# Optimization experiments

Hardware: AMD Instinct MI355X
Metric: run time of the kernel (lower is better)

## Reference

```python
import jax, jax.numpy as jnp
import numpy as np

BS, HIST, H, W, NOBJ = 512, 3, 10, 10, 4
NSENT, TOK, DM = 3, 36, 768
EMB, FM, K, NL, ADIM = 256, 64, 2, 128, 5
LIN = FM * (H - (K - 1)) * (W - (K - 1))  # 64*9*9 = 5184
ATTN_SCALE = float(np.sqrt(EMB))  # 16.0


def setup_inputs() -> dict:
    key = jax.random.key(0)
    ks = jax.random.split(key, 24)
    g = lambda i, shape, s=0.02: jax.random.normal(ks[i], shape, dtype=jnp.float32) * s
    sprite_emb = g(0, (25, EMB), 1.0).at[0].set(0.0)  # padding_idx=0 -> zero row
    inp = {
        'state': jax.random.randint(ks[1], (BS, HIST, H, W, NOBJ), 0, 25, dtype=jnp.int32),
        'action': jax.random.randint(ks[2], (BS,), 0, ADIM, dtype=jnp.int32),
        'temb': jax.random.normal(ks[3], (BS, NSENT, TOK, DM), dtype=jnp.float32),
        'sprite_emb': sprite_emb,
        'conv_w': g(4, (K, K, HIST * EMB, FM)),  # HWIO
        'conv_b': g(5, (FM,)),
        'Wk': g(6, (DM, EMB)), 'bk': g(7, (EMB,)),
        'Wks': g(8, (DM, 1)), 'bks': g(9, (1,)),
        'Wv': g(10, (DM, EMB)), 'bv': g(11, (EMB,)),
        'Wvs': g(12, (DM, 1)), 'bvs': g(13, (1,)),
        'a1': g(14, (LIN, NL)), 'a1b': g(15, (NL,)),
        'a2': g(16, (NL, NL)), 'a2b': g(17, (NL,)),
        'a3': g(18, (NL, ADIM)), 'a3b': g(19, (ADIM,)),
        'v1': g(20, (LIN, NL)), 'v1b': g(21, (NL,)),
        'v2': g(22, (NL, NL)), 'v2b': g(23, (NL,)),
        'v3': jax.random.normal(jax.random.fold_in(key, 99), (NL, 1)) * 0.02,
        'v3b': jnp.zeros((1,), jnp.float32),
    }
    return inp


def _nonzero_mean(e):
    # e: [..., n, emb]; mean over rows that are nonzero (padding rows are all-zero)
    cnt = jnp.sum(jnp.sum(e, axis=-1) != 0, axis=-1, keepdims=True)
    return jnp.sum(e, axis=-2) / jnp.maximum(cnt, 1).astype(e.dtype)


def reference(state, action, temb, sprite_emb, conv_w, conv_b, Wk, bk, Wks, bks,
              Wv, bv, Wvs, bvs, a1, a1b, a2, a2b, a3, a3b, v1, v1b, v2, v2b, v3, v3b):
    lrelu = jax.nn.leaky_relu  # slope 0.01 matches torch default
    bs = state.shape[0]
    obj_state, avt_state = state[..., :-1], state[..., -1:]
    query = _nonzero_mean(sprite_emb[obj_state])   # [bs,hist,H,W,emb]
    avatar = _nonzero_mean(sprite_emb[avt_state])  # [bs,hist,H,W,emb]
    # text key/value: scaled token-softmax pooling over tokens (dim=2)
    k = (temb @ Wk + bk) * jax.nn.softmax(temb @ Wks + bks, axis=-2)
    k = jnp.sum(k, axis=2)                          # [bs,nsent,emb]
    v = (temb @ Wv + bv) * jax.nn.softmax(temb @ Wvs + bvs, axis=-2)
    v = jnp.sum(v, axis=2)                          # [bs,nsent,emb]
    # batch_attention
    q2 = query.reshape(bs, -1, EMB)                 # [bs, hist*H*W, emb]
    kq = jnp.einsum('bxe,bse->bxs', q2, k) / ATTN_SCALE
    wts = jax.nn.softmax(kq, axis=-1) * (kq != 0)
    wts = wts.reshape(bs, HIST, H, W, NSENT)
    # mean(weights[...,None]*value, dim=-2) == (w @ v) / nsent
    att = jnp.einsum('bthws,bse->bthwe', wts, v) / NSENT  # [bs,hist,H,W,emb]
    st = att.reshape(bs, H, W, -1)                  # fold hist into channels (768)
    av = avatar.reshape(bs, H, W, -1)
    st = (st + av) / 2.0                            # NHWC, C=768
    y = jax.lax.conv_general_dilated(st, conv_w, (1, 1), 'VALID',
                                     dimension_numbers=('NHWC', 'HWIO', 'NHWC')) + conv_b
    y = lrelu(y)                                    # [bs,9,9,64]
    y = jnp.transpose(y, (0, 3, 1, 2)).reshape(bs, -1)  # torch NCHW flatten order
    ha = lrelu(lrelu(y @ a1 + a1b) @ a2 + a2b)
    logits = ha @ a3 + a3b
    logp = jax.nn.log_softmax(logits, axis=-1)
    action_logprobs = jnp.take_along_axis(logp, action[:, None].astype(jnp.int32), axis=-1)[:, 0]
    entropy = -jnp.sum(jnp.exp(logp) * logp, axis=-1)
    hv = lrelu(lrelu(y @ v1 + v1b) @ v2 + v2b)
    state_value = (hv @ v3 + v3b)[:, 0]
    return action_logprobs, state_value, entropy
```

## Files before the change

kernel.cpp:

```cpp
#include <hip/hip_runtime.h>
#include <hip/hip_bf16.h>
#include <math.h>

constexpr int BS   = 512;
constexpr int DM   = 768;
constexpr int NBS  = 1536;
constexpr int NPOS = 300;
constexpr int LIN  = 5184;
constexpr int KSPLIT = 9, KCH = 576;
constexpr int NROW = 55296;

typedef __attribute__((ext_vector_type(8))) short bf16x8;
typedef __attribute__((ext_vector_type(4))) short s16x4;
typedef __attribute__((ext_vector_type(4))) float f32x4;

static __device__ __forceinline__ short f2bf(float f) {
    unsigned u = __float_as_uint(f);
    unsigned r = (u + 0x7FFFu + ((u >> 16) & 1u)) >> 16;
    return (short)r;
}
static __device__ __forceinline__ float bf2f_lo(unsigned u) { return __uint_as_float(u << 16); }
static __device__ __forceinline__ float bf2f_hi(unsigned u) { return __uint_as_float(u & 0xFFFF0000u); }

constexpr size_t OFF_RD   = 0;
constexpr size_t OFF_FL   = 19968;
constexpr size_t OFF_DT   = 20032;
constexpr size_t OFF_W2T  = 118336;
constexpr size_t OFF_WVH  = 167488;
constexpr size_t OFF_WCT  = 216640;
constexpr size_t OFF_PH   = 511552;
constexpr size_t OFF_AB   = 536128;
constexpr size_t OFF_SK   = 1199680;
constexpr size_t OFF_SV   = 1254976;
constexpr size_t OFF_XKH  = 1310272;
constexpr size_t OFF_XVH  = 1900096;
constexpr size_t OFF_VWH  = 2489920;
constexpr size_t OFF_YH   = 3079744;
constexpr size_t OFF_PART = 4406848;

__global__ __launch_bounds__(256) void k1_scores_prep(
    const float* __restrict__ temb, const float* __restrict__ Wks,
    const float* __restrict__ Wvs, const float* __restrict__ conv_w,
    const float* __restrict__ sprite, const float* __restrict__ Wk,
    const float* __restrict__ Wv, const float* __restrict__ bv,
    const float* __restrict__ a1, const float* __restrict__ v1,
    float* __restrict__ SK, float* __restrict__ SV,
    short* __restrict__ W2T, short* __restrict__ WVH, short* __restrict__ AB,
    short* __restrict__ PH, float* __restrict__ RD, int* __restrict__ FL)
{
    __shared__ float tile[64][65];
    int tid = threadIdx.x, bx = blockIdx.x;

    if (bx < 13824) {
        int wid = tid >> 6, lane = tid & 63;
        size_t r = (size_t)bx * 4 + wid;
        const float4* row = (const float4*)temb + r * 192;
        const float4* k4 = (const float4*)Wks;
        const float4* v4 = (const float4*)Wvs;
        float pk = 0.f, pv = 0.f;
        #pragma unroll
        for (int i = 0; i < 3; ++i) {
            int d4 = lane + 64 * i;
            float4 x = row[d4];
            float4 wk = k4[d4], wv = v4[d4];
            pk += x.x * wk.x + x.y * wk.y + x.z * wk.z + x.w * wk.w;
            pv += x.x * wv.x + x.y * wv.y + x.z * wv.z + x.w * wv.w;
        }
        #pragma unroll
        for (int off = 32; off; off >>= 1) {
            pk += __shfl_down(pk, off);
            pv += __shfl_down(pv, off);
        }
        if (lane == 0) { SK[r] = pk; SV[r] = pv; }
        return;
    }

    int id = bx - 13824;
    if (id < 48) {
        int p = id >> 2, cq = id & 3;
        int t4 = p / 3, j = p - t4 * 3;
        int c0 = cq * 64;
        #pragma unroll
        for (int it = 0; it < 16; ++it) {
            int idx = it * 256 + tid; int ci = idx >> 6, f = idx & 63;
            tile[ci][f] = conv_w[(size_t)(t4 * 768 + j * 256 + c0 + ci) * 64 + f];
        }
        __syncthreads();
        #pragma unroll
        for (int it = 0; it < 16; ++it) {
            int idx = it * 256 + tid; int f = idx >> 6, ci = idx & 63;
            W2T[(size_t)((t4 * 3 + j) * 64 + f) * 256 + c0 + ci] = f2bf(tile[ci][f]);
        }
    } else if (id < 96) {
        int b2 = id - 48;
        int base = b2 * 4096 + tid * 16;
        #pragma unroll
        for (int q = 0; q < 4; ++q) {
            float4 v = *(const float4*)(Wv + base + q * 4);
            s16x4 h = { f2bf(v.x), f2bf(v.y), f2bf(v.z), f2bf(v.w) };
            *(s16x4*)(WVH + base + q * 4) = h;
        }
    } else if (id < 420) {
        int q = id - 96; int kt = q % 81, nt = q / 81;
        const float* src = (nt < 2) ? a1 : v1;
        int col0 = (nt & 1) * 64;
        #pragma unroll
        for (int it = 0; it < 16; ++it) {
            int idx = it * 256 + tid; int ki = idx >> 6, ni = idx & 63;
            tile[ki][ni] = src[(size_t)(kt * 64 + ki) * 128 + col0 + ni];
        }
        __syncthreads();
        #pragma unroll
        for (int it = 0; it < 16; ++it) {
            int idx = it * 256 + tid; int ni = idx >> 6, ki = idx & 63;
            AB[(size_t)(nt * 64 + ni) * 5184 + kt * 64 + ki] = f2bf(tile[ki][ni]);
        }
    } else if (id < 495) {
        int g = (id - 420) * 256 + tid;
        int o = g / 768, d = g - o * 768;
        const float* sp = sprite + o * 256;
        const float* wr = Wk + (size_t)d * 256;
        float s = 0.f;
        for (int c = 0; c < 256; ++c) s += sp[c] * wr[c];
        PH[(size_t)o * 768 + d] = f2bf(s);
    } else if (id < 573) {
        int g = (id - 495) * 256 + tid;
        int o = g / 768, n = g - o * 768;
        int tap = n >> 6, f = n & 63; int t4 = tap / 3, j = tap - t4 * 3;
        const float* sp = (o < 25) ? (sprite + o * 256) : bv;
        float s = 0.f;
        for (int e = 0; e < 256; ++e)
            s += sp[e] * conv_w[(size_t)(t4 * 768 + j * 256 + e) * 64 + f];
        RD[g] = s;
    } else {
        if (tid < 25) {
            float s = 0.f;
            for (int c = 0; c < 256; ++c) s += sprite[tid * 256 + c];
            FL[tid] = (s != 0.0f) ? 1 : 0;
        }
    }
}

__global__ __launch_bounds__(384) void kB2_sum(
    const float* __restrict__ temb, const float* __restrict__ SK,
    const float* __restrict__ SV, short* __restrict__ XKH, short* __restrict__ XVH)
{
    __shared__ float swk[40], swv[40];
    int tid = threadIdx.x, bs = blockIdx.x;
    int wid = tid >> 6, lane = tid & 63;

    if (wid < 2) {
        const float* S = wid ? SV : SK;
        float s = (lane < 36) ? S[(size_t)bs * 36 + lane] : -INFINITY;
        float m = s;
        #pragma unroll
        for (int off = 32; off; off >>= 1) m = fmaxf(m, __shfl_xor(m, off));
        float e = (lane < 36) ? expf(s - m) : 0.f;
        float z = e;
        #pragma unroll
        for (int off = 32; off; off >>= 1) z += __shfl_xor(z, off);
        float* dst = wid ? swv : swk;
        if (lane < 36) dst[lane] = e / z;
    }
    __syncthreads();

    const float2* row = (const float2*)(temb + (size_t)bs * 27648);
    float k0 = 0.f, k1 = 0.f, v0 = 0.f, v1 = 0.f;
    #pragma unroll
    for (int t = 0; t < 36; ++t) {
        float2 x = row[(size_t)t * 384 + tid];
        float wk = swk[t], wv = swv[t];
        k0 += wk * x.x; k1 += wk * x.y;
        v0 += wv * x.x; v1 += wv * x.y;
    }
    ushort2 hk = { (unsigned short)f2bf(k0), (unsigned short)f2bf(k1) };
    ushort2 hv = { (unsigned short)f2bf(v0), (unsigned short)f2bf(v1) };
    *(ushort2*)&XKH[(size_t)bs * 768 + 2 * tid] = hk;
    *(ushort2*)&XVH[(size_t)bs * 768 + 2 * tid] = hv;
}

template<int BIAS, int OUTBF>
__global__ __launch_bounds__(256) void gemm_mfma(
    const short* __restrict__ A, const short* __restrict__ B,
    const float* __restrict__ bias, void* __restrict__ Cout,
    int K, int ldc, int klen, size_t czstride)
{
    __shared__ short As[64][40];
    __shared__ short Bs[64][40];
    int tid = threadIdx.x;
    int bm = blockIdx.x * 64, bn = blockIdx.y * 64;
    int wid = tid >> 6, lane = tid & 63;
    int wm = (wid >> 1) * 32, wn = (wid & 1) * 32;
    int l15 = lane & 15, lg = lane >> 4;

    f32x4 zero = {0.f, 0.f, 0.f, 0.f};
    f32x4 acc00 = zero, acc01 = zero, acc10 = zero, acc11 = zero;

    int srow = tid >> 2, kch = (tid & 3) * 8;
    const short* Ap = A + (size_t)(bm + srow) * K + kch + (size_t)blockIdx.z * klen;
    const short* Bp = B + (size_t)(bn + srow) * K + kch + (size_t)blockIdx.z * klen;

    for (int kt = 0; kt < klen; kt += 32) {
        bf16x8 aval = *(const bf16x8*)(Ap + kt);
        bf16x8 bval = *(const bf16x8*)(Bp + kt);
        *(bf16x8*)&As[srow][kch] = aval;
        *(bf16x8*)&Bs[srow][kch] = bval;
        __syncthreads();
        bf16x8 af0 = *(const bf16x8*)&As[wm + l15][lg * 8];
        bf16x8 af1 = *(const bf16x8*)&As[wm + 16 + l15][lg * 8];
        bf16x8 bg0 = *(const bf16x8*)&Bs[wn + l15][lg * 8];
        bf16x8 bg1 = *(const bf16x8*)&Bs[wn + 16 + l15][lg * 8];
        acc00 = __builtin_amdgcn_mfma_f32_16x16x32_bf16(af0, bg0, acc00, 0, 0, 0);
        acc01 = __builtin_amdgcn_mfma_f32_16x16x32_bf16(af0, bg1, acc01, 0, 0, 0);
        acc10 = __builtin_amdgcn_mfma_f32_16x16x32_bf16(af1, bg0, acc10, 0, 0, 0);
        acc11 = __builtin_amdgcn_mfma_f32_16x16x32_bf16(af1, bg1, acc11, 0, 0, 0);
        __syncthreads();
    }

    float* Cf = (float*)Cout + (size_t)blockIdx.z * czstride;
    short* Ch = (short*)Cout;
    #pragma unroll
    for (int i = 0; i < 2; ++i) {
        f32x4 arow0 = (i == 0) ? acc00 : acc10;
        f32x4 arow1 = (i == 0) ? acc01 : acc11;
        #pragma unroll
        for (int j = 0; j < 2; ++j) {
            f32x4 a = (j == 0) ? arow0 : arow1;
            int col = bn + wn + j * 16 + l15;
            float bb = BIAS ? bias[col] : 0.f;
            #pragma unroll
            for (int r = 0; r < 4; ++r) {
                int row = bm + wm + i * 16 + lg * 4 + r;
                float v = a[r] + bb;
                if (OUTBF) Ch[(size_t)row * ldc + col] = f2bf(v);
                else       Cf[(size_t)row * ldc + col] = v;
            }
        }
    }
}

__global__ __launch_bounds__(256) void k3_vwdt(
    const short* __restrict__ XVH, const short* __restrict__ WCT,
    const float* __restrict__ bvW2, short* __restrict__ VWH,
    const short* __restrict__ XKH, const short* __restrict__ PH,
    float* __restrict__ DT)
{
    __shared__ short As[64][40];
    __shared__ short Bs[64][40];
    int tid = threadIdx.x;
    bool isdt = (blockIdx.y == 12);
    const short* A = isdt ? XKH : XVH;
    const short* B = isdt ? PH  : WCT;
    int bm = blockIdx.x * 64, bn = isdt ? 0 : blockIdx.y * 64;
    int wid = tid >> 6, lane = tid & 63;
    int wm = (wid >> 1) * 32, wn = (wid & 1) * 32;
    int l15 = lane & 15, lg = lane >> 4;

    f32x4 zero = {0.f, 0.f, 0.f, 0.f};
    f32x4 acc00 = zero, acc01 = zero, acc10 = zero, acc11 = zero;

    int srow = tid >> 2, kch = (tid & 3) * 8;
    const short* Ap = A + (size_t)(bm + srow) * 768 + kch;
    const short* Bp = B + (size_t)(bn + srow) * 768 + kch;

    for (int kt = 0; kt < 768; kt += 32) {
        bf16x8 aval = *(const bf16x8*)(Ap + kt);
        bf16x8 bval = *(const bf16x8*)(Bp + kt);
        *(bf16x8*)&As[srow][kch] = aval;
        *(bf16x8*)&Bs[srow][kch] = bval;
        __syncthreads();
        bf16x8 af0 = *(const bf16x8*)&As[wm + l15][lg * 8];
        bf16x8 af1 = *(const bf16x8*)&As[wm + 16 + l15][lg * 8];
        bf16x8 bg0 = *(const bf16x8*)&Bs[wn + l15][lg * 8];
        bf16x8 bg1 = *(const bf16x8*)&Bs[wn + 16 + l15][lg * 8];
        acc00 = __builtin_amdgcn_mfma_f32_16x16x32_bf16(af0, bg0, acc00, 0, 0, 0);
        acc01 = __builtin_amdgcn_mfma_f32_16x16x32_bf16(af0, bg1, acc01, 0, 0, 0);
        acc10 = __builtin_amdgcn_mfma_f32_16x16x32_bf16(af1, bg0, acc10, 0, 0, 0);
        acc11 = __builtin_amdgcn_mfma_f32_16x16x32_bf16(af1, bg1, acc11, 0, 0, 0);
        __syncthreads();
    }

    #pragma unroll
    for (int i = 0; i < 2; ++i) {
        f32x4 arow0 = (i == 0) ? acc00 : acc10;
        f32x4 arow1 = (i == 0) ? acc01 : acc11;
        #pragma unroll
        for (int j = 0; j < 2; ++j) {
            f32x4 a = (j == 0) ? arow0 : arow1;
            int col = bn + wn + j * 16 + l15;
            #pragma unroll
            for (int r = 0; r < 4; ++r) {
                int row = bm + wm + i * 16 + lg * 4 + r;
                if (isdt) DT[(size_t)row * 64 + col] = a[r];
                else      VWH[(size_t)row * 768 + col] = f2bf(a[r] + bvW2[col]);
            }
        }
    }
}

__global__ __launch_bounds__(512) void k4_y(
    const int* __restrict__ state, const float* __restrict__ dt,
    const int* __restrict__ flags, const short* __restrict__ VWH,
    const float* __restrict__ rowdot, const float* __restrict__ conv_b,
    short* __restrict__ y)
{
    int b = blockIdx.x, tid = threadIdx.x;
    __shared__ float s_vW[3 * 768];
    __shared__ float s_w[3][NPOS + 4];
    __shared__ int   s_avt[NPOS + 4];
    __shared__ float s_y[81 * 65];

    const unsigned* vr = (const unsigned*)(VWH + (size_t)b * 3 * 768);
    for (int i = tid; i < 1152; i += 512) {
        unsigned u = vr[i];
        s_vW[2 * i]     = bf2f_lo(u);
        s_vW[2 * i + 1] = bf2f_hi(u);
    }

    for (int code = tid; code < NPOS; code += 512) {
        const int* st = state + ((size_t)b * NPOS + code) * 4;
        int o0 = st[0], o1 = st[1], o2 = st[2], avi = st[3];
        int cnt = flags[o0] + flags[o1] + flags[o2];
        s_avt[code] = avi;
        float w0 = 0.f, w1 = 0.f, w2 = 0.f;
        if (cnt > 0) {
            const float* d0 = dt + (size_t)b * 192;
            float inv = 1.0f / (16.0f * (float)cnt);
            float q0 = (d0[o0]       + d0[o1]       + d0[o2])       * inv;
            float q1 = (d0[64 + o0]  + d0[64 + o1]  + d0[64 + o2])  * inv;
            float q2 = (d0[128 + o0] + d0[128 + o1] + d0[128 + o2]) * inv;
            float m = fmaxf(q0, fmaxf(q1, q2));
            float e0 = expf(q0 - m), e1 = expf(q1 - m), e2 = expf(q2 - m);
            float is = 1.0f / (6.0f * (e0 + e1 + e2));
            w0 = e0 * is; w1 = e1 * is; w2 = e2 * is;
        }
        s_w[0][code] = w0; s_w[1][code] = w1; s_w[2][code] = w2;
    }
    __syncthreads();

    int f = tid & 63;
    float cb = conv_b[f];
    for (int p = tid >> 6; p < 81; p += 8) {
        int oh = p / 9, ow = p - oh * 9;
        float acc = cb;
        #pragma unroll
        for (int kh = 0; kh < 2; ++kh)
        #pragma unroll
        for (int kw = 0; kw < 2; ++kw) {
            int bc = 3 * ((oh + kh) * 10 + (ow + kw));
            int tbase = ((kh * 2 + kw) * 3) * 64 + f;
            #pragma unroll
            for (int j = 0; j < 3; ++j) {
                int code = bc + j;
                int tf = tbase + j * 64;
                acc += s_w[0][code] * s_vW[tf]
                     + s_w[1][code] * s_vW[768 + tf]
                     + s_w[2][code] * s_vW[2 * 768 + tf];
                acc += 0.5f * rowdot[(size_t)s_avt[code] * 768 + tf];
            }
        }
        acc = acc > 0.f ? acc : 0.01f * acc;
        s_y[p * 65 + f] = acc;
    }
    __syncthreads();
    for (int i = tid; i < LIN; i += 512) {
        int ff = i / 81, pp = i - ff * 81;
        y[(size_t)b * LIN + i] = f2bf(s_y[pp * 65 + ff]);
    }
}

__global__ __launch_bounds__(128) void k6_heads(
    const float* __restrict__ PART, const float* __restrict__ a1b,
    const float* __restrict__ v1b, const int* __restrict__ action,
    const float* __restrict__ a2, const float* __restrict__ a2b,
    const float* __restrict__ a3, const float* __restrict__ a3b,
    const float* __restrict__ v2, const float* __restrict__ v2b,
    const float* __restrict__ v3, const float* __restrict__ v3b,
    float* __restrict__ out)
{
    int b = blockIdx.x, tid = threadIdx.x;
    __shared__ float h1a[128], h1v[128], h2a[128], red[128];
    __shared__ float lg[5];
    float sa0 = a1b[tid], sv0 = v1b[tid];
    const float* pb = PART + (size_t)b * 256;
    for (int z = 0; z < KSPLIT; ++z) {
        sa0 += pb[(size_t)z * (BS * 256) + tid];
        sv0 += pb[(size_t)z * (BS * 256) + 128 + tid];
    }
    h1a[tid] = sa0 > 0.f ? sa0 : 0.01f * sa0;
    h1v[tid] = sv0 > 0.f ? sv0 : 0.01f * sv0;
    __syncthreads();
    float sa = a2b[tid], sv = v2b[tid];
    for (int k = 0; k < 128; ++k) {
        sa += h1a[k] * a2[k * 128 + tid];
        sv += h1v[k] * v2[k * 128 + tid];
    }
    sa = sa > 0.f ? sa : 0.01f * sa;
    sv = sv > 0.f ? sv : 0.01f * sv;
    h2a[tid] = sa;
    red[tid] = sv * v3[tid];
    __syncthreads();
    for (int s = 64; s > 0; s >>= 1) {
        if (tid < s) red[tid] += red[tid + s];
        __syncthreads();
    }
    if (tid < 5) {
        float l = a3b[tid];
        for (int k = 0; k < 128; ++k) l += h2a[k] * a3[k * 5 + tid];
        lg[tid] = l;
    }
    __syncthreads();
    if (tid == 0) {
        float m = lg[0];
        for (int j2 = 1; j2 < 5; ++j2) m = fmaxf(m, lg[j2]);
        float se = 0.f;
        for (int j2 = 0; j2 < 5; ++j2) se += expf(lg[j2] - m);
        float lse = m + logf(se);
        int act = action[b];
        float ent = 0.f;
        for (int j2 = 0; j2 < 5; ++j2) {
            float lp = lg[j2] - lse;
            ent -= expf(lp) * lp;
        }
        out[b]        = lg[act] - lse;
        out[512 + b]  = red[0] + v3b[0];
        out[1024 + b] = ent;
    }
}

extern "C" void kernel_launch(void* const* d_in, const int* in_sizes, int n_in,
                              void* d_out, int out_size, void* d_ws, size_t ws_size,
                              hipStream_t stream)
{
    const int*   state  = (const int*)d_in[0];
    const int*   action = (const int*)d_in[1];
    const float* temb   = (const float*)d_in[2];
    const float* sprite = (const float*)d_in[3];
    const float* conv_w = (const float*)d_in[4];
    const float* conv_b = (const float*)d_in[5];
    const float* Wk     = (const float*)d_in[6];
    const float* Wks    = (const float*)d_in[8];
    const float* Wv     = (const float*)d_in[10];
    const float* bv     = (const float*)d_in[11];
    const float* Wvs    = (const float*)d_in[12];
    const float* a1     = (const float*)d_in[14];
    const float* a1b    = (const float*)d_in[15];
    const float* a2     = (const float*)d_in[16];
    const float* a2b    = (const float*)d_in[17];
    const float* a3     = (const float*)d_in[18];
    const float* a3b    = (const float*)d_in[19];
    const float* v1     = (const float*)d_in[20];
    const float* v1b    = (const float*)d_in[21];
    const float* v2     = (const float*)d_in[22];
    const float* v2b    = (const float*)d_in[23];
    const float* v3     = (const float*)d_in[24];
    const float* v3b    = (const float*)d_in[25];
    (void)in_sizes; (void)n_in; (void)out_size; (void)ws_size;

    float* ws  = (float*)d_ws;
    float* RD  = ws + OFF_RD;
    float* bvW2= RD + 25 * 768;
    int*   FL  = (int*)(ws + OFF_FL);
    float* DT  = ws + OFF_DT;
    short* W2T = (short*)(ws + OFF_W2T);
    short* WVH = (short*)(ws + OFF_WVH);
    short* WCT = (short*)(ws + OFF_WCT);
    short* PH  = (short*)(ws + OFF_PH);
    short* AB  = (short*)(ws + OFF_AB);
    float* SK  = ws + OFF_SK;
    float* SV  = ws + OFF_SV;
    short* XKH = (short*)(ws + OFF_XKH);
    short* XVH = (short*)(ws + OFF_XVH);
    short* VWH = (short*)(ws + OFF_VWH);
    short* YH  = (short*)(ws + OFF_YH);
    float* PART= ws + OFF_PART;
    float* out = (float*)d_out;

    k1_scores_prep<<<13824 + 574, 256, 0, stream>>>(
        temb, Wks, Wvs, conv_w, sprite, Wk, Wv, bv, a1, v1,
        SK, SV, W2T, WVH, AB, PH, RD, FL);
    kB2_sum<<<NBS, 384, 0, stream>>>(temb, SK, SV, XKH, XVH);
    gemm_mfma<0,1><<<dim3(12,12,1),256,0,stream>>>(W2T, WVH, nullptr, WCT, 256, 768, 256, 0);
    k3_vwdt<<<dim3(24,13,1),256,0,stream>>>(XVH, WCT, bvW2, VWH, XKH, PH, DT);
    k4_y<<<BS, 512, 0, stream>>>(state, DT, FL, VWH, RD, conv_b, YH);
    gemm_mfma<0,0><<<dim3(8,4,KSPLIT),256,0,stream>>>(YH, AB, nullptr, PART, 5184, 256, KCH, (size_t)BS*256);
    k6_heads<<<BS, 128, 0, stream>>>(PART, a1b, v1b, action, a2, a2b, a3, a3b,
                                     v2, v2b, v3, v3b, out);
}
```

Baseline: 131.0 us.

## Fold conv-weight x Wv product into prep kernel and split softmax from token sum

Drops the separate bf16 transpose and cast of conv_w and Wv and the small MFMA GEMM that formed WCT. WCT is now computed directly in fp32 by extra blocks of the prep kernel using an LDS-tiled scalar GEMM, which removes one launch and two staging buffers. The token softmax moves into its own small kernel that writes the weights to global memory. The token-weighted sum then uses float4 loads over 192 threads with batched loads. This trades one launch for another and replaces MFMA with scalar FMA for WCT, which could lengthen the tail of the prep kernel.

```diff
diff --git a/kernel.cpp b/kernel.cpp
--- a/kernel.cpp
+++ b/kernel.cpp
@@ -3,15 +3,12 @@
 #include <math.h>
 
 constexpr int BS   = 512;
-constexpr int DM   = 768;
 constexpr int NBS  = 1536;
 constexpr int NPOS = 300;
 constexpr int LIN  = 5184;
 constexpr int KSPLIT = 9, KCH = 576;
-constexpr int NROW = 55296;
 
 typedef __attribute__((ext_vector_type(8))) short bf16x8;
-typedef __attribute__((ext_vector_type(4))) short s16x4;
 typedef __attribute__((ext_vector_type(4))) float f32x4;
 
 static __device__ __forceinline__ short f2bf(float f) {
@@ -19,34 +16,37 @@
     unsigned r = (u + 0x7FFFu + ((u >> 16) & 1u)) >> 16;
     return (short)r;
 }
+static __device__ __forceinline__ unsigned pk2(float a, float b) {
+    return ((unsigned)(unsigned short)f2bf(a)) | (((unsigned)(unsigned short)f2bf(b)) << 16);
+}
 static __device__ __forceinline__ float bf2f_lo(unsigned u) { return __uint_as_float(u << 16); }
 static __device__ __forceinline__ float bf2f_hi(unsigned u) { return __uint_as_float(u & 0xFFFF0000u); }
 
 constexpr size_t OFF_RD   = 0;
 constexpr size_t OFF_FL   = 19968;
 constexpr size_t OFF_DT   = 20032;
-constexpr size_t OFF_W2T  = 118336;
-constexpr size_t OFF_WVH  = 167488;
-constexpr size_t OFF_WCT  = 216640;
-constexpr size_t OFF_PH   = 511552;
-constexpr size_t OFF_AB   = 536128;
-constexpr size_t OFF_SK   = 1199680;
-constexpr size_t OFF_SV   = 1254976;
-constexpr size_t OFF_XKH  = 1310272;
-constexpr size_t OFF_XVH  = 1900096;
-constexpr size_t OFF_VWH  = 2489920;
-constexpr size_t OFF_YH   = 3079744;
-constexpr size_t OFF_PART = 4406848;
-
-__global__ __launch_bounds__(256) void k1_scores_prep(
+constexpr size_t OFF_WCT  = 118336;
+constexpr size_t OFF_PH   = 413248;
+constexpr size_t OFF_AB   = 437824;
+constexpr size_t OFF_SK   = 1101376;
+constexpr size_t OFF_SV   = 1156672;
+constexpr size_t OFF_SWK  = 1211968;
+constexpr size_t OFF_SWV  = 1267264;
+constexpr size_t OFF_XKH  = 1322560;
+constexpr size_t OFF_XVH  = 1912384;
+constexpr size_t OFF_VWH  = 2502208;
+constexpr size_t OFF_YH   = 3092032;
+constexpr size_t OFF_PART = 4419136;
+
+__global__ __launch_bounds__(256) void kS_scores_prep(
     const float* __restrict__ temb, const float* __restrict__ Wks,
     const float* __restrict__ Wvs, const float* __restrict__ conv_w,
     const float* __restrict__ sprite, const float* __restrict__ Wk,
     const float* __restrict__ Wv, const float* __restrict__ bv,
     const float* __restrict__ a1, const float* __restrict__ v1,
     float* __restrict__ SK, float* __restrict__ SV,
-    short* __restrict__ W2T, short* __restrict__ WVH, short* __restrict__ AB,
-    short* __restrict__ PH, float* __restrict__ RD, int* __restrict__ FL)
+    short* __restrict__ AB, short* __restrict__ PH, short* __restrict__ WCT,
+    float* __restrict__ RD, int* __restrict__ FL)
 {
     __shared__ float tile[64][65];
     int tid = threadIdx.x, bx = blockIdx.x;
@@ -76,32 +76,8 @@
     }
 
     int id = bx - 13824;
-    if (id < 48) {
-        int p = id >> 2, cq = id & 3;
-        int t4 = p / 3, j = p - t4 * 3;
-        int c0 = cq * 64;
-        #pragma unroll
-        for (int it = 0; it < 16; ++it) {
-            int idx = it * 256 + tid; int ci = idx >> 6, f = idx & 63;
-            tile[ci][f] = conv_w[(size_t)(t4 * 768 + j * 256 + c0 + ci) * 64 + f];
-        }
-        __syncthreads();
-        #pragma unroll
-        for (int it = 0; it < 16; ++it) {
-            int idx = it * 256 + tid; int f = idx >> 6, ci = idx & 63;
-            W2T[(size_t)((t4 * 3 + j) * 64 + f) * 256 + c0 + ci] = f2bf(tile[ci][f]);
-        }
-    } else if (id < 96) {
-        int b2 = id - 48;
-        int base = b2 * 4096 + tid * 16;
-        #pragma unroll
-        for (int q = 0; q < 4; ++q) {
-            float4 v = *(const float4*)(Wv + base + q * 4);
-            s16x4 h = { f2bf(v.x), f2bf(v.y), f2bf(v.z), f2bf(v.w) };
-            *(s16x4*)(WVH + base + q * 4) = h;
-        }
-    } else if (id < 420) {
-        int q = id - 96; int kt = q % 81, nt = q / 81;
+    if (id < 324) {
+        int kt = id % 81, nt = id / 81;
         const float* src = (nt < 2) ? a1 : v1;
         int col0 = (nt & 1) * 64;
         #pragma unroll
@@ -115,23 +91,70 @@
             int idx = it * 256 + tid; int ni = idx >> 6, ki = idx & 63;
             AB[(size_t)(nt * 64 + ni) * 5184 + kt * 64 + ki] = f2bf(tile[ki][ni]);
         }
-    } else if (id < 495) {
-        int g = (id - 420) * 256 + tid;
-        int o = g / 768, d = g - o * 768;
-        const float* sp = sprite + o * 256;
-        const float* wr = Wk + (size_t)d * 256;
-        float s = 0.f;
-        for (int c = 0; c < 256; ++c) s += sp[c] * wr[c];
-        PH[(size_t)o * 768 + d] = f2bf(s);
-    } else if (id < 573) {
-        int g = (id - 495) * 256 + tid;
-        int o = g / 768, n = g - o * 768;
-        int tap = n >> 6, f = n & 63; int t4 = tap / 3, j = tap - t4 * 3;
-        const float* sp = (o < 25) ? (sprite + o * 256) : bv;
-        float s = 0.f;
-        for (int e = 0; e < 256; ++e)
-            s += sp[e] * conv_w[(size_t)(t4 * 768 + j * 256 + e) * 64 + f];
-        RD[g] = s;
+    } else if (id < 399) {
+        int g = (id - 324) * 256 + tid;
+        if (g < 19200) {
+            int o = g / 768, d = g - o * 768;
+            const float* sp = sprite + o * 256;
+            const float* wr = Wk + (size_t)d * 256;
+            float s = 0.f;
+            for (int c = 0; c < 256; ++c) s += sp[c] * wr[c];
+            PH[(size_t)o * 768 + d] = f2bf(s);
+        }
+    } else if (id < 477) {
+        int g = (id - 399) * 256 + tid;
+        if (g < 19968) {
+            int o = g / 768, n = g - o * 768;
+            int tap = n >> 6, f = n & 63; int t4 = tap / 3, j = tap - t4 * 3;
+            const float* sp = (o < 25) ? (sprite + o * 256) : bv;
+            float s = 0.f;
+            for (int e = 0; e < 256; ++e)
+                s += sp[e] * conv_w[(size_t)(t4 * 768 + j * 256 + e) * 64 + f];
+            RD[g] = s;
+        }
+    } else if (id < 621) {
+        int wid2 = id - 477;
+        int bm = (wid2 / 12) * 64, bn = (wid2 % 12) * 64;
+        int p = bm >> 6; int t4 = p / 3, jj = p - t4 * 3;
+        const float* cwb = conv_w + (size_t)(t4 * 768 + jj * 256) * 64;
+        float* As = (float*)tile;
+        float* Bs = (float*)tile + 2080;
+        float acc[4][4];
+        #pragma unroll
+        for (int i = 0; i < 4; ++i)
+            #pragma unroll
+            for (int j = 0; j < 4; ++j) acc[i][j] = 0.f;
+        int tm = tid >> 4, tn = tid & 15;
+        for (int kc = 0; kc < 256; kc += 32) {
+            #pragma unroll
+            for (int it = 0; it < 8; ++it) {
+                int idx = it * 256 + tid; int c = idx >> 6, f = idx & 63;
+                As[c * 65 + f] = cwb[(size_t)(kc + c) * 64 + f];
+            }
+            #pragma unroll
+            for (int it = 0; it < 8; ++it) {
+                int idx = it * 256 + tid; int d = idx >> 5, c = idx & 31;
+                Bs[c * 65 + d] = Wv[(size_t)(bn + d) * 256 + kc + c];
+            }
+            __syncthreads();
+            for (int kk = 0; kk < 32; ++kk) {
+                float a[4], b[4];
+                #pragma unroll
+                for (int i = 0; i < 4; ++i) a[i] = As[kk * 65 + tm * 4 + i];
+                #pragma unroll
+                for (int j = 0; j < 4; ++j) b[j] = Bs[kk * 65 + tn * 4 + j];
+                #pragma unroll
+                for (int i = 0; i < 4; ++i)
+                    #pragma unroll
+                    for (int j = 0; j < 4; ++j) acc[i][j] += a[i] * b[j];
+            }
+            __syncthreads();
+        }
+        #pragma unroll
+        for (int i = 0; i < 4; ++i)
+            #pragma unroll
+            for (int j = 0; j < 4; ++j)
+                WCT[(size_t)(bm + tm * 4 + i) * 768 + bn + tn * 4 + j] = f2bf(acc[i][j]);
     } else {
         if (tid < 25) {
             float s = 0.f;
@@ -141,17 +164,14 @@
     }
 }
 
-__global__ __launch_bounds__(384) void kB2_sum(
-    const float* __restrict__ temb, const float* __restrict__ SK,
-    const float* __restrict__ SV, short* __restrict__ XKH, short* __restrict__ XVH)
-{
-    __shared__ float swk[40], swv[40];
-    int tid = threadIdx.x, bs = blockIdx.x;
-    int wid = tid >> 6, lane = tid & 63;
-
-    if (wid < 2) {
-        const float* S = wid ? SV : SK;
-        float s = (lane < 36) ? S[(size_t)bs * 36 + lane] : -INFINITY;
+__global__ __launch_bounds__(512) void kW_weights(
+    const float* __restrict__ SK, const float* __restrict__ SV,
+    float* __restrict__ SWK, float* __restrict__ SWV)
+{
+    int w = threadIdx.x >> 6, lane = threadIdx.x & 63;
+    int bs = blockIdx.x * 8 + w;
+    {
+        float s = (lane < 36) ? SK[(size_t)bs * 36 + lane] : -1e30f;
         float m = s;
         #pragma unroll
         for (int off = 32; off; off >>= 1) m = fmaxf(m, __shfl_xor(m, off));
@@ -159,24 +179,53 @@
         float z = e;
         #pragma unroll
         for (int off = 32; off; off >>= 1) z += __shfl_xor(z, off);
-        float* dst = wid ? swv : swk;
-        if (lane < 36) dst[lane] = e / z;
-    }
+        if (lane < 36) SWK[(size_t)bs * 36 + lane] = e / z;
+    }
+    {
+        float s = (lane < 36) ? SV[(size_t)bs * 36 + lane] : -1e30f;
+        float m = s;
+        #pragma unroll
+        for (int off = 32; off; off >>= 1) m = fmaxf(m, __shfl_xor(m, off));
+        float e = (lane < 36) ? expf(s - m) : 0.f;
+        float z = e;
+        #pragma unroll
+        for (int off = 32; off; off >>= 1) z += __shfl_xor(z, off);
+        if (lane < 36) SWV[(size_t)bs * 36 + lane] = e / z;
+    }
+}
+
+__global__ __launch_bounds__(192) void kX_sum(
+    const float* __restrict__ temb, const float* __restrict__ SWK,
+    const float* __restrict__ SWV, short* __restrict__ XKH, short* __restrict__ XVH)
+{
+    __shared__ float sw[72];
+    int tid = threadIdx.x, bs = blockIdx.x;
+    if (tid < 36) sw[tid] = SWK[(size_t)bs * 36 + tid];
+    else if (tid >= 64 && tid < 100) sw[tid - 28] = SWV[(size_t)bs * 36 + tid - 64];
     __syncthreads();
 
-    const float2* row = (const float2*)(temb + (size_t)bs * 27648);
-    float k0 = 0.f, k1 = 0.f, v0 = 0.f, v1 = 0.f;
+    const float4* row4 = (const float4*)temb + (size_t)bs * 6912;
+    float k0 = 0.f, k1 = 0.f, k2 = 0.f, k3 = 0.f;
+    float v0 = 0.f, v1 = 0.f, v2 = 0.f, v3 = 0.f;
     #pragma unroll
-    for (int t = 0; t < 36; ++t) {
-        float2 x = row[(size_t)t * 384 + tid];
-        float wk = swk[t], wv = swv[t];
-        k0 += wk * x.x; k1 += wk * x.y;
-        v0 += wv * x.x; v1 += wv * x.y;
-    }
-    ushort2 hk = { (unsigned short)f2bf(k0), (unsigned short)f2bf(k1) };
-    ushort2 hv = { (unsigned short)f2bf(v0), (unsigned short)f2bf(v1) };
-    *(ushort2*)&XKH[(size_t)bs * 768 + 2 * tid] = hk;
-    *(ushort2*)&XVH[(size_t)bs * 768 + 2 * tid] = hv;
+    for (int b = 0; b < 3; ++b) {
+        float4 xv[12];
+        #pragma unroll
+        for (int j = 0; j < 12; ++j) xv[j] = row4[(size_t)(b * 12 + j) * 192 + tid];
+        #pragma unroll
+        for (int j = 0; j < 12; ++j) {
+            int t = b * 12 + j;
+            float wk = sw[t], wv = sw[36 + t];
+            k0 += wk * xv[j].x; k1 += wk * xv[j].y;
+            k2 += wk * xv[j].z; k3 += wk * xv[j].w;
+            v0 += wv * xv[j].x; v1 += wv * xv[j].y;
+            v2 += wv * xv[j].z; v3 += wv * xv[j].w;
+        }
+    }
+    uint2 hk = { pk2(k0, k1), pk2(k2, k3) };
+    uint2 hv = { pk2(v0, v1), pk2(v2, v3) };
+    ((uint2*)XKH)[(size_t)bs * 192 + tid] = hk;
+    ((uint2*)XVH)[(size_t)bs * 192 + tid] = hv;
 }
 
 template<int BIAS, int OUTBF>
@@ -462,13 +511,13 @@
     float* bvW2= RD + 25 * 768;
     int*   FL  = (int*)(ws + OFF_FL);
     float* DT  = ws + OFF_DT;
-    short* W2T = (short*)(ws + OFF_W2T);
-    short* WVH = (short*)(ws + OFF_WVH);
     short* WCT = (short*)(ws + OFF_WCT);
     short* PH  = (short*)(ws + OFF_PH);
     short* AB  = (short*)(ws + OFF_AB);
     float* SK  = ws + OFF_SK;
     float* SV  = ws + OFF_SV;
+    float* SWK = ws + OFF_SWK;
+    float* SWV = ws + OFF_SWV;
     short* XKH = (short*)(ws + OFF_XKH);
     short* XVH = (short*)(ws + OFF_XVH);
     short* VWH = (short*)(ws + OFF_VWH);
@@ -476,11 +525,11 @@
     float* PART= ws + OFF_PART;
     float* out = (float*)d_out;
 
-    k1_scores_prep<<<13824 + 574, 256, 0, stream>>>(
+    kS_scores_prep<<<13824 + 622, 256, 0, stream>>>(
         temb, Wks, Wvs, conv_w, sprite, Wk, Wv, bv, a1, v1,
-        SK, SV, W2T, WVH, AB, PH, RD, FL);
-    kB2_sum<<<NBS, 384, 0, stream>>>(temb, SK, SV, XKH, XVH);
-    gemm_mfma<0,1><<<dim3(12,12,1),256,0,stream>>>(W2T, WVH, nullptr, WCT, 256, 768, 256, 0);
+        SK, SV, AB, PH, WCT, RD, FL);
+    kW_weights<<<192, 512, 0, stream>>>(SK, SV, SWK, SWV);
+    kX_sum<<<NBS, 192, 0, stream>>>(temb, SWK, SWV, XKH, XVH);
     k3_vwdt<<<dim3(24,13,1),256,0,stream>>>(XVH, WCT, bvW2, VWH, XKH, PH, DT);
     k4_y<<<BS, 512, 0, stream>>>(state, DT, FL, VWH, RD, conv_b, YH);
     gemm_mfma<0,0><<<dim3(8,4,KSPLIT),256,0,stream>>>(YH, AB, nullptr, PART, 5184, 256, KCH, (size_t)BS*256);
```

After: 137.7 us. 5.1% more time.
